# Optimization experiments

Hardware: AMD Instinct MI355X
Metric: run time of the kernel (lower is better)

Reference implementation:

```python
import jax, jax.numpy as jnp
import numpy as np

B = 16384
IN = 256
OUT = 256
NUM_CELLS = 4
TOPK = 2


def setup_inputs() -> dict:
    key = jax.random.key(0)
    ks = jax.random.split(key, 7)
    d = IN + OUT
    return {
        "x": jax.random.normal(ks[0], (B, IN), jnp.float32),
        "c": jax.random.normal(ks[1], (B, OUT), jnp.float32),
        "h": jax.random.normal(ks[2], (B, OUT), jnp.float32),
        "W_gates": jax.random.normal(ks[3], (d, 4 * OUT * NUM_CELLS), jnp.float32) / np.sqrt(d),
        "b_gates": jnp.zeros((4 * OUT * NUM_CELLS,), jnp.float32),
        "W_ctrl": jax.random.normal(ks[4], (d, NUM_CELLS), jnp.float32) / np.sqrt(d),
        "b_ctrl": jnp.zeros((NUM_CELLS,), jnp.float32),
    }


def top_k_softmax(logits, k, n):
    # topk(k+1) then slice to k, matching the torch code
    top_vals, top_idx = jax.lax.top_k(logits, min(k + 1, n))
    probs = jax.nn.softmax(top_vals[:, :k], axis=-1)
    b = logits.shape[0]
    gate = jnp.zeros((b, n), logits.dtype)
    gate = gate.at[jnp.arange(b)[:, None], top_idx[:, :k]].add(probs)
    return gate


def reference(x, c, h, W_gates, b_gates, W_ctrl, b_ctrl):
    feats = jnp.concatenate([x, h], axis=-1)              # [B, IN+OUT]
    logits = feats @ W_ctrl + b_ctrl                      # [B, N]
    gate = top_k_softmax(logits, TOPK, NUM_CELLS)         # [B, N] sparse top-k probs
    combined = feats @ W_gates + b_gates                  # [B, 4*OUT*N]
    combined = combined.reshape(-1, NUM_CELLS, 4, OUT)    # [B, N, 4, OUT]
    i = jax.nn.sigmoid(combined[:, :, 0])
    j = combined[:, :, 1]
    f = jax.nn.sigmoid(combined[:, :, 2])
    o = jax.nn.sigmoid(combined[:, :, 3])
    new_c = f * c[:, None, :] + i * jnp.tanh(j)           # [B, N, OUT]
    new_h = o * jnp.tanh(new_c)                           # [B, N, OUT]
    nc = jnp.einsum('bn,bno->bo', gate, new_c)            # routed combine
    nh = jnp.einsum('bn,bno->bo', gate, new_h)
    return (nh, nc)
```

## Files before the change

kernel.cpp:

```cpp
#include <hip/hip_runtime.h>
#include <hip/hip_bf16.h>

#define NB 16384
#define DD 512
#define NCOLS 4096

typedef __attribute__((ext_vector_type(8))) short short8;
typedef __attribute__((ext_vector_type(4))) float f32x4;

__device__ __forceinline__ float sigmoidf_(float x) {
    float e = __builtin_amdgcn_exp2f(-1.442695041f * x);
    return __builtin_amdgcn_rcpf(1.f + e);
}
__device__ __forceinline__ float tanhf_(float x) {
    float e = __builtin_amdgcn_exp2f(-2.885390082f * x);
    return 2.f * __builtin_amdgcn_rcpf(1.f + e) - 1.f;
}

#define GLOAD_LDS16(g, l) __builtin_amdgcn_global_load_lds( \
    (__attribute__((address_space(1))) void*)(g), \
    (__attribute__((address_space(3))) void*)(l), 16, 0, 0)

__global__ void k_pre(const float* __restrict__ x, const float* __restrict__ h,
                      const float* __restrict__ Wc, const float* __restrict__ bc,
                      const float* __restrict__ Wg,
                      __hip_bfloat16* __restrict__ featsB, float* __restrict__ gates,
                      __hip_bfloat16* __restrict__ W4, int* __restrict__ counts) {
    int bid = blockIdx.x;
    if (bid == 0 && threadIdx.x < 6) counts[threadIdx.x] = 0;
    if (bid < 4096) {
        int wave = bid * 4 + (threadIdx.x >> 6);
        int lane = threadIdx.x & 63;
        int row = wave;
        int k0 = lane * 8;
        const float* src = (k0 < 256) ? (x + (size_t)row * 256 + k0)
                                      : (h + (size_t)row * 256 + k0 - 256);
        float4 f0 = ((const float4*)src)[0];
        float4 f1 = ((const float4*)src)[1];
        float fv[8] = {f0.x, f0.y, f0.z, f0.w, f1.x, f1.y, f1.z, f1.w};
        __hip_bfloat16 tmp[8];
#pragma unroll
        for (int j = 0; j < 8; ++j) tmp[j] = __float2bfloat16(fv[j]);
        *reinterpret_cast<short8*>(featsB + (size_t)row * 512 + k0) =
            *reinterpret_cast<short8*>(tmp);
        float acc[4] = {0.f, 0.f, 0.f, 0.f};
#pragma unroll
        for (int j = 0; j < 8; ++j) {
            float4 w = ((const float4*)Wc)[k0 + j];
            acc[0] += fv[j] * w.x; acc[1] += fv[j] * w.y;
            acc[2] += fv[j] * w.z; acc[3] += fv[j] * w.w;
        }
#pragma unroll
        for (int off = 32; off; off >>= 1) {
#pragma unroll
            for (int c = 0; c < 4; ++c) acc[c] += __shfl_xor(acc[c], off);
        }
        if (lane == 0) {
            float l[4];
#pragma unroll
            for (int c = 0; c < 4; ++c) l[c] = acc[c] + bc[c];
            int i1 = 0;
#pragma unroll
            for (int c = 1; c < 4; ++c) if (l[c] > l[i1]) i1 = c;
            int i2 = -1;
#pragma unroll
            for (int c = 0; c < 4; ++c)
                if (c != i1 && (i2 < 0 || l[c] > l[i2])) i2 = c;
            float e = __expf(l[i2] - l[i1]);
            float p1 = 1.f / (1.f + e);
            float p2 = e / (1.f + e);
            float g[4] = {0.f, 0.f, 0.f, 0.f};
            g[i1] = p1; g[i2] = p2;
            float4 gv; gv.x = g[0]; gv.y = g[1]; gv.z = g[2]; gv.w = g[3];
            *(float4*)(gates + (size_t)row * 4) = gv;
        }
    } else {
        int c = (bid - 4096) * 256 + threadIdx.x;
        int lane = c & 63;
        int kkg  = (c >> 6) & 15;
        int rowg = (c >> 10) & 7;
        int ob   = (c >> 13) & 7;
        int cell = c >> 16;
        int oi = lane & 15, hi = lane >> 4;
        int gate = rowg & 3, oh = rowg >> 2;
        int col = cell * 1024 + gate * 256 + ob * 32 + oh * 16 + oi;
        int kb = kkg * 32 + hi * 8;
        __hip_bfloat16 tmp[8];
#pragma unroll
        for (int j = 0; j < 8; ++j)
            tmp[j] = __float2bfloat16(Wg[(size_t)(kb + j) * 4096 + col]);
        *reinterpret_cast<short8*>(W4 + (size_t)c * 8) = *reinterpret_cast<short8*>(tmp);
    }
}

__global__ void k_bucket(const float* __restrict__ gates, int* __restrict__ counts,
                         int* __restrict__ rowList) {
    __shared__ int wcnt[4][6];
    __shared__ int wbase[4][6];
    int tid = threadIdx.x;
    int wave = tid >> 6, lane = tid & 63;
    int row = blockIdx.x * 256 + tid;
    float4 g = *(const float4*)(gates + (size_t)row * 4);
    int i1 = 0; float m1 = g.x;
    if (g.y > m1) { m1 = g.y; i1 = 1; }
    if (g.z > m1) { m1 = g.z; i1 = 2; }
    if (g.w > m1) { m1 = g.w; i1 = 3; }
    int i2 = -1; float m2 = -1.f;
    if (i1 != 0)             { m2 = g.x; i2 = 0; }
    if (i1 != 1 && g.y > m2) { m2 = g.y; i2 = 1; }
    if (i1 != 2 && g.z > m2) { m2 = g.z; i2 = 2; }
    if (i1 != 3 && g.w > m2) { m2 = g.w; i2 = 3; }
    int a = min(i1, i2), b = max(i1, i2);
    int pid = (a == 0) ? (b - 1) : (a == 1) ? (1 + b) : 5;
    int pre = 0;
#pragma unroll
    for (int q = 0; q < 6; ++q) {
        unsigned long long m = __ballot(pid == q);
        if (pid == q) pre = __popcll(m & ((1ull << lane) - 1ull));
        if (lane == 0) wcnt[wave][q] = __popcll(m);
    }
    __syncthreads();
    if (tid < 6) {
        int q = tid;
        int t0 = wcnt[0][q], t1 = wcnt[1][q], t2 = wcnt[2][q], t3 = wcnt[3][q];
        int tot = t0 + t1 + t2 + t3;
        int base = (tot > 0) ? atomicAdd(counts + q, tot) : 0;
        wbase[0][q] = base;
        wbase[1][q] = base + t0;
        wbase[2][q] = base + t0 + t1;
        wbase[3][q] = base + t0 + t1 + t2;
    }
    __syncthreads();
    rowList[pid * 16384 + wbase[wave][pid] + pre] = row;
}

__launch_bounds__(256, 3)
__global__ void k_main(const __hip_bfloat16* __restrict__ featsB,
                       const __hip_bfloat16* __restrict__ W4,
                       const float* __restrict__ cin,
                       const float* __restrict__ gates,
                       const float* __restrict__ bg,
                       const int* __restrict__ counts,
                       const int* __restrict__ rowList,
                       float* __restrict__ out) {
    __shared__ char smem[25600];
    float* oAcc  = (float*)smem;
    float* cinS  = (float*)(smem + 16384);
    float* gatesS = (float*)(smem + 24576);

    int tid = threadIdx.x;
    int wave = tid >> 6, lane = tid & 63;
    int wc = wave;
    int hi = lane >> 4, lsw = lane & 7, l15 = lane & 15;

    int lin = blockIdx.x;
    int r_ = lin & 7;
    int v_ = lin >> 3;
    int ob = v_ & 7;
    int bq = r_ + ((v_ >> 3) << 3);

    int c0_ = counts[0], c1_ = counts[1], c2_ = counts[2],
        c3_ = counts[3], c4_ = counts[4], c5_ = counts[5];
    int s1 = (c0_ + 63) >> 6;
    int s2 = s1 + ((c1_ + 63) >> 6);
    int s3 = s2 + ((c2_ + 63) >> 6);
    int s4 = s3 + ((c3_ + 63) >> 6);
    int s5 = s4 + ((c4_ + 63) >> 6);
    int total = s5 + ((c5_ + 63) >> 6);
    if (bq >= total) return;
    int p, chunk, cnt, cA, cB;
    if      (bq < s1) { p = 0; chunk = bq;      cnt = c0_; cA = 0; cB = 1; }
    else if (bq < s2) { p = 1; chunk = bq - s1; cnt = c1_; cA = 0; cB = 2; }
    else if (bq < s3) { p = 2; chunk = bq - s2; cnt = c2_; cA = 0; cB = 3; }
    else if (bq < s4) { p = 3; chunk = bq - s3; cnt = c3_; cA = 1; cB = 2; }
    else if (bq < s5) { p = 4; chunk = bq - s4; cnt = c4_; cA = 1; cB = 3; }
    else              { p = 5; chunk = bq - s5; cnt = c5_; cA = 2; cB = 3; }
    int nvalid = min(64, cnt - chunk * 64);
    int rowbase = p * 16384 + chunk * 64;

    int ohh = wc & 1;
    int ch  = wc >> 1;
    int cell = ch ? cB : cA;

    int e0 = tid,        rA0 = e0 >> 3, gA0 = (e0 & 7) ^ (rA0 & 7);
    int e1 = 256 + tid,  rA1 = e1 >> 3, gA1 = (e1 & 7) ^ (rA1 & 7);
    int grA0 = rowList[rowbase + ((rA0 < nvalid) ? rA0 : 0)];
    int grA1 = rowList[rowbase + ((rA1 < nvalid) ? rA1 : 0)];
    const __hip_bfloat16* sA0 = featsB + (size_t)grA0 * 512 + gA0 * 8;
    const __hip_bfloat16* sA1 = featsB + (size_t)grA1 * 512 + gA1 * 8;
    int dA0 = e0 * 16, dA1 = e1 * 16;

    const __hip_bfloat16* bBw =
        W4 + ((size_t)(cell * 8 + ob) * 128 + ohh * 64) * 512 + lane * 8;

    f32x4 acc[4][4];
#pragma unroll
    for (int m = 0; m < 4; ++m)
#pragma unroll
        for (int n = 0; n < 4; ++n)
            acc[m][n] = (f32x4){0.f, 0.f, 0.f, 0.f};

    short8 br[2][4][2];

#define STAGE_A(kt_, buf_) do { \
        GLOAD_LDS16(sA0 + (kt_) * 64, smem + (buf_) * 8192 + dA0); \
        GLOAD_LDS16(sA1 + (kt_) * 64, smem + (buf_) * 8192 + dA1); \
    } while (0)
#define LOAD_B(pb_, kt_) do { \
        _Pragma("unroll") \
        for (int n_ = 0; n_ < 4; ++n_) \
            _Pragma("unroll") \
            for (int kk_ = 0; kk_ < 2; ++kk_) \
                br[pb_][n_][kk_] = *reinterpret_cast<const short8*>( \
                    bBw + n_ * 8192 + ((kt_) * 2 + kk_) * 512); \
    } while (0)

    STAGE_A(0, 0);
    {
        int ec0 = tid,       rc0 = ec0 >> 3, qc0 = ec0 & 7;
        int ec1 = 256 + tid, rc1 = ec1 >> 3, qc1 = ec1 & 7;
        int gr0 = rowList[rowbase + ((rc0 < nvalid) ? rc0 : 0)];
        int gr1 = rowList[rowbase + ((rc1 < nvalid) ? rc1 : 0)];
        GLOAD_LDS16(cin + (size_t)gr0 * 256 + ob * 32 + qc0 * 4,
                    (char*)cinS + ec0 * 16);
        GLOAD_LDS16(cin + (size_t)gr1 * 256 + ob * 32 + qc1 * 4,
                    (char*)cinS + ec1 * 16);
        if (tid < 64) {
            int gr = rowList[rowbase + ((tid < nvalid) ? tid : 0)];
            GLOAD_LDS16(gates + (size_t)gr * 4, (char*)gatesS + tid * 16);
        }
    }
    LOAD_B(0, 0);
    __syncthreads();

#pragma unroll
    for (int kt = 0; kt < 8; ++kt) {
        const int buf = kt & 1;
        if (kt < 7) {
            STAGE_A(kt + 1, buf ^ 1);
            LOAD_B(buf ^ 1, kt + 1);
        }
        const char* Ab = smem + buf * 8192;
#pragma unroll
        for (int kk = 0; kk < 2; ++kk) {
            short8 fa[4];
#pragma unroll
            for (int m = 0; m < 4; ++m) {
                int row = m * 16 + l15;
                int chunkc = (kk * 4 + hi) ^ lsw;
                fa[m] = *reinterpret_cast<const short8*>(Ab + row * 128 + chunkc * 16);
            }
#pragma unroll
            for (int m = 0; m < 4; ++m)
#pragma unroll
                for (int n = 0; n < 4; ++n)
                    acc[m][n] = __builtin_amdgcn_mfma_f32_16x16x32_bf16(
                        fa[m], br[buf][n][kk], acc[m][n], 0, 0, 0);
        }
        __syncthreads();
    }
#undef STAGE_A
#undef LOAD_B

    int og = ob * 32 + ohh * 16 + l15;
    float bb0 = bg[cell * 1024 + 0 * 256 + og];
    float bb1 = bg[cell * 1024 + 1 * 256 + og];
    float bb2 = bg[cell * 1024 + 2 * 256 + og];
    float bb3 = bg[cell * 1024 + 3 * 256 + og];

#define LSTM_BODY(STORE_OP) \
    _Pragma("unroll") \
    for (int m = 0; m < 4; ++m) { \
        _Pragma("unroll") \
        for (int reg = 0; reg < 4; ++reg) { \
            int r = m * 16 + hi * 4 + reg; \
            float gw = gatesS[r * 4 + cell]; \
            float iv = sigmoidf_(acc[m][0][reg] + bb0); \
            float jv = acc[m][1][reg] + bb1; \
            float fv = sigmoidf_(acc[m][2][reg] + bb2); \
            float ov = sigmoidf_(acc[m][3][reg] + bb3); \
            float cv = cinS[r * 32 + ohh * 16 + l15]; \
            float ncl = fv * cv + iv * tanhf_(jv); \
            float nhl = ov * tanhf_(ncl); \
            oAcc[r * 32 + ohh * 16 + l15] STORE_OP gw * nhl; \
            oAcc[2048 + r * 32 + ohh * 16 + l15] STORE_OP gw * ncl; \
        } \
    }

    if (ch == 0) { LSTM_BODY(=) }
    __syncthreads();
    if (ch == 1) { LSTM_BODY(+=) }
    __syncthreads();
#undef LSTM_BODY

    {
        int r = tid >> 2, q = tid & 3;
        if (r < nvalid) {
            int grow = rowList[rowbase + r];
            size_t obase = (size_t)grow * 256 + ob * 32 + q * 8;
            *(float4*)&out[obase]     = *(float4*)&oAcc[r * 32 + q * 8];
            *(float4*)&out[obase + 4] = *(float4*)&oAcc[r * 32 + q * 8 + 4];
            *(float4*)&out[(size_t)NB * 256 + obase]     = *(float4*)&oAcc[2048 + r * 32 + q * 8];
            *(float4*)&out[(size_t)NB * 256 + obase + 4] = *(float4*)&oAcc[2048 + r * 32 + q * 8 + 4];
        }
    }
}

extern "C" void kernel_launch(void* const* d_in, const int* in_sizes, int n_in,
                              void* d_out, int out_size, void* d_ws, size_t ws_size,
                              hipStream_t stream) {
    const float* x  = (const float*)d_in[0];
    const float* c  = (const float*)d_in[1];
    const float* h  = (const float*)d_in[2];
    const float* Wg = (const float*)d_in[3];
    const float* bg = (const float*)d_in[4];
    const float* Wc = (const float*)d_in[5];
    const float* bc = (const float*)d_in[6];
    float* out = (float*)d_out;

    const size_t featsB_bytes = (size_t)NB * DD * 2;
    const size_t w4_bytes     = (size_t)NCOLS * DD * 2;
    const size_t gates_bytes  = (size_t)NB * 4 * 4;
    const size_t counts_bytes = 256;
    const size_t rlist_bytes  = (size_t)6 * 16384 * 4;
    if (ws_size < featsB_bytes + w4_bytes + gates_bytes + counts_bytes + rlist_bytes)
        return;

    char* ws = (char*)d_ws;
    __hip_bfloat16* featsB = (__hip_bfloat16*)ws;
    __hip_bfloat16* W4     = (__hip_bfloat16*)(ws + featsB_bytes);
    float*          gatesW = (float*)(ws + featsB_bytes + w4_bytes);
    int*            counts = (int*)(ws + featsB_bytes + w4_bytes + gates_bytes);
    int*            rowLst = (int*)(ws + featsB_bytes + w4_bytes + gates_bytes + counts_bytes);

    k_pre<<<dim3(5120), dim3(256), 0, stream>>>(x, h, Wc, bc, Wg, featsB, gatesW,
                                                W4, counts);
    k_bucket<<<dim3(64), dim3(256), 0, stream>>>(gatesW, counts, rowLst);
    k_main<<<dim3(2176), dim3(256), 0, stream>>>(featsB, W4, c, gatesW, bg,
                                                 counts, rowLst, out);
}
```

Before: 82.88 us.

## Double K-tile depth to 128 and split B register prefetch into halves

Widens each K step from 64 to 128, so the A tile in LDS doubles to 16KB per buffer and the main loop runs 4 iterations instead of 8, halving the barrier count. B fragments are now prefetched in two half-tiles that are interleaved with the MFMA halves, which keeps the register footprint similar. LDS use grows to about 41KB per block, which may limit how many blocks fit per CU under the launch bound of 3.

Measured after the change: 84.41 us. No clear change (+1.8%).

```diff
diff --git a/kernel.cpp b/kernel.cpp
--- a/kernel.cpp
+++ b/kernel.cpp
@@ -143,10 +143,10 @@
                        const int* __restrict__ counts,
                        const int* __restrict__ rowList,
                        float* __restrict__ out) {
-    __shared__ char smem[25600];
+    __shared__ char smem[41984];
     float* oAcc  = (float*)smem;
-    float* cinS  = (float*)(smem + 16384);
-    float* gatesS = (float*)(smem + 24576);
+    float* cinS  = (float*)(smem + 32768);
+    float* gatesS = (float*)(smem + 40960);
 
     int tid = threadIdx.x;
     int wave = tid >> 6, lane = tid & 63;
@@ -182,13 +182,15 @@
     int ch  = wc >> 1;
     int cell = ch ? cB : cA;
 
-    int e0 = tid,        rA0 = e0 >> 3, gA0 = (e0 & 7) ^ (rA0 & 7);
-    int e1 = 256 + tid,  rA1 = e1 >> 3, gA1 = (e1 & 7) ^ (rA1 & 7);
-    int grA0 = rowList[rowbase + ((rA0 < nvalid) ? rA0 : 0)];
-    int grA1 = rowList[rowbase + ((rA1 < nvalid) ? rA1 : 0)];
-    const __hip_bfloat16* sA0 = featsB + (size_t)grA0 * 512 + gA0 * 8;
-    const __hip_bfloat16* sA1 = featsB + (size_t)grA1 * 512 + gA1 * 8;
-    int dA0 = e0 * 16, dA1 = e1 * 16;
+    int t16 = tid >> 4;
+    int cswA = (tid & 15) ^ (t16 & 7);
+    const __hip_bfloat16* sA[4];
+#pragma unroll
+    for (int q = 0; q < 4; ++q) {
+        int rq = q * 16 + t16;
+        int grq = rowList[rowbase + ((rq < nvalid) ? rq : 0)];
+        sA[q] = featsB + (size_t)grq * 512 + cswA * 8;
+    }
 
     const __hip_bfloat16* bBw =
         W4 + ((size_t)(cell * 8 + ob) * 128 + ohh * 64) * 512 + lane * 8;
@@ -200,19 +202,46 @@
         for (int n = 0; n < 4; ++n)
             acc[m][n] = (f32x4){0.f, 0.f, 0.f, 0.f};
 
-    short8 br[2][4][2];
+    short8 br01[4][2];
+    short8 br23[4][2];
 
 #define STAGE_A(kt_, buf_) do { \
-        GLOAD_LDS16(sA0 + (kt_) * 64, smem + (buf_) * 8192 + dA0); \
-        GLOAD_LDS16(sA1 + (kt_) * 64, smem + (buf_) * 8192 + dA1); \
+        _Pragma("unroll") \
+        for (int q_ = 0; q_ < 4; ++q_) \
+            GLOAD_LDS16(sA[q_] + (kt_) * 128, \
+                        smem + (buf_) * 16384 + (q_ * 256 + tid) * 16); \
     } while (0)
-#define LOAD_B(pb_, kt_) do { \
-        _Pragma("unroll") \
-        for (int n_ = 0; n_ < 4; ++n_) \
+#define LOAD_B01(kt_) do { \
+        _Pragma("unroll") \
+        for (int n_ = 0; n_ < 4; ++n_) { \
+            br01[n_][0] = *reinterpret_cast<const short8*>(bBw + n_ * 8192 + ((kt_) * 4 + 0) * 512); \
+            br01[n_][1] = *reinterpret_cast<const short8*>(bBw + n_ * 8192 + ((kt_) * 4 + 1) * 512); \
+        } \
+    } while (0)
+#define LOAD_B23(kt_) do { \
+        _Pragma("unroll") \
+        for (int n_ = 0; n_ < 4; ++n_) { \
+            br23[n_][0] = *reinterpret_cast<const short8*>(bBw + n_ * 8192 + ((kt_) * 4 + 2) * 512); \
+            br23[n_][1] = *reinterpret_cast<const short8*>(bBw + n_ * 8192 + ((kt_) * 4 + 3) * 512); \
+        } \
+    } while (0)
+#define MFMA_HALF(BR_, kkbase_, Ab_) do { \
+        _Pragma("unroll") \
+        for (int kk_ = 0; kk_ < 2; ++kk_) { \
+            short8 fa_[4]; \
             _Pragma("unroll") \
-            for (int kk_ = 0; kk_ < 2; ++kk_) \
-                br[pb_][n_][kk_] = *reinterpret_cast<const short8*>( \
-                    bBw + n_ * 8192 + ((kt_) * 2 + kk_) * 512); \
+            for (int m_ = 0; m_ < 4; ++m_) { \
+                int row_ = m_ * 16 + l15; \
+                int chunkc_ = (((kkbase_) + kk_) * 4 + hi) ^ lsw; \
+                fa_[m_] = *reinterpret_cast<const short8*>((Ab_) + row_ * 256 + chunkc_ * 16); \
+            } \
+            _Pragma("unroll") \
+            for (int m_ = 0; m_ < 4; ++m_) \
+                _Pragma("unroll") \
+                for (int n_ = 0; n_ < 4; ++n_) \
+                    acc[m_][n_] = __builtin_amdgcn_mfma_f32_16x16x32_bf16( \
+                        fa_[m_], BR_[n_][kk_], acc[m_][n_], 0, 0, 0); \
+        } \
     } while (0)
 
     STAGE_A(0, 0);
@@ -230,37 +259,24 @@
             GLOAD_LDS16(gates + (size_t)gr * 4, (char*)gatesS + tid * 16);
         }
     }
-    LOAD_B(0, 0);
-    __syncthreads();
-
-#pragma unroll
-    for (int kt = 0; kt < 8; ++kt) {
+    LOAD_B01(0);
+    __syncthreads();
+
+#pragma unroll
+    for (int kt = 0; kt < 4; ++kt) {
         const int buf = kt & 1;
-        if (kt < 7) {
-            STAGE_A(kt + 1, buf ^ 1);
-            LOAD_B(buf ^ 1, kt + 1);
-        }
-        const char* Ab = smem + buf * 8192;
-#pragma unroll
-        for (int kk = 0; kk < 2; ++kk) {
-            short8 fa[4];
-#pragma unroll
-            for (int m = 0; m < 4; ++m) {
-                int row = m * 16 + l15;
-                int chunkc = (kk * 4 + hi) ^ lsw;
-                fa[m] = *reinterpret_cast<const short8*>(Ab + row * 128 + chunkc * 16);
-            }
-#pragma unroll
-            for (int m = 0; m < 4; ++m)
-#pragma unroll
-                for (int n = 0; n < 4; ++n)
-                    acc[m][n] = __builtin_amdgcn_mfma_f32_16x16x32_bf16(
-                        fa[m], br[buf][n][kk], acc[m][n], 0, 0, 0);
-        }
+        if (kt < 3) STAGE_A(kt + 1, buf ^ 1);
+        LOAD_B23(kt);
+        const char* Ab = smem + buf * 16384;
+        MFMA_HALF(br01, 0, Ab);
+        if (kt < 3) LOAD_B01(kt + 1);
+        MFMA_HALF(br23, 2, Ab);
         __syncthreads();
     }
 #undef STAGE_A
-#undef LOAD_B
+#undef LOAD_B01
+#undef LOAD_B23
+#undef MFMA_HALF
 
     int og = ob * 32 + ohh * 16 + l15;
     float bb0 = bg[cell * 1024 + 0 * 256 + og];
```
